# Optimization experiments

Hardware: AMD Instinct MI355X
Metric: run time of the kernel (lower is better)

## Reference

```python
import jax, jax.numpy as jnp
import numpy as np

N, T, D, C = 32, 512, 1024, 120
EPS = 1e-12
SCALE = 2.0 * (D ** 0.5)


def setup_inputs() -> dict:
    key = jax.random.key(0)
    ks = jax.random.split(key, 16)
    inp = {
        'anc_perm_input': jax.random.normal(ks[0], (N, T, D), dtype=jnp.float32),
        'pos_perm_input': jax.random.normal(ks[1], (N, T, D), dtype=jnp.float32),
        'neg_perm_input': jax.random.normal(ks[2], (N, T, D), dtype=jnp.float32),
        'anc_src_key_padding_mask': jax.random.randint(ks[3], (N, T), 0, 2) == 1,
        'pos_src_key_padding_mask': jax.random.randint(ks[4], (N, T), 0, 2) == 1,
        'neg_src_key_padding_mask': jax.random.randint(ks[5], (N, T), 0, 2) == 1,
        # learned parameters (stored as (in, out); math-equivalent to torch x @ W.T)
        'W_attn': jax.random.normal(ks[6], (D, D), dtype=jnp.float32) * 0.02,
        'b_attn': jnp.zeros((D,), dtype=jnp.float32),
        'W1': jax.random.normal(ks[7], (D, D), dtype=jnp.float32) * 0.02,
        'b1': jnp.zeros((D,), dtype=jnp.float32),
        'W2': jax.random.normal(ks[8], (D, D), dtype=jnp.float32) * 0.02,
        'b2': jnp.zeros((D,), dtype=jnp.float32),
        'ln_g': jnp.ones((D,), dtype=jnp.float32),
        'ln_b': jnp.zeros((D,), dtype=jnp.float32),
        'W_last': jax.random.normal(ks[9], (D, C), dtype=jnp.float32) * 0.02,
        'b_last': jnp.zeros((C,), dtype=jnp.float32),
    }
    return inp


def _ntd_nd(x, mask, W_attn, b_attn, W1, b1, W2, b2, ln_g, ln_b, W_last, b_last):
    # x: (N,T,D); mask: (N,T) bool, True = padding
    w = x @ W_attn + b_attn                                   # (N,T,D)
    valid = ~mask                                             # (N,T)
    scores = jnp.einsum('btd,bsd->bts', w, w)                 # (N,T,T)
    scores = jnp.where(valid[:, :, None] & valid[:, None, :], scores, 0.0)
    s = jnp.sum(scores, axis=1) / SCALE                       # (N,T)
    s = jnp.where(mask, -jnp.inf, s)
    attn = jax.nn.softmax(s, axis=1)                          # (N,T)
    # proj_head: duplicate OrderedDict key => linear1 -> relu -> linear2 (no final act)
    proj = jax.nn.relu(x @ W1 + b1) @ W2 + b2                 # (N,T,D)
    pooled = jnp.einsum('bt,btd->bd', attn, proj)             # (N,D)
    mu = jnp.mean(pooled, axis=-1, keepdims=True)
    var = jnp.var(pooled, axis=-1, keepdims=True)
    normed = (pooled - mu) / jnp.sqrt(var + EPS) * ln_g + ln_b
    return jax.nn.relu(normed) @ W_last + b_last              # (N,C)


def reference(anc_perm_input, pos_perm_input, neg_perm_input,
              anc_src_key_padding_mask, pos_src_key_padding_mask, neg_src_key_padding_mask,
              W_attn, b_attn, W1, b1, W2, b2, ln_g, ln_b, W_last, b_last):
    params = (W_attn, b_attn, W1, b1, W2, b2, ln_g, ln_b, W_last, b_last)
    anc = _ntd_nd(anc_perm_input, anc_src_key_padding_mask, *params)
    pos = _ntd_nd(pos_perm_input, pos_src_key_padding_mask, *params)
    neg = _ntd_nd(neg_perm_input, neg_src_key_padding_mask, *params)
    return (anc, pos, neg)
```

## Files before the change

kernel.cpp:

```cpp
#include <hip/hip_runtime.h>
#include <hip/hip_bf16.h>
#include <math.h>

#define N_B 32
#define T_S 512
#define D_D 1024
#define C_C 120
#define ZB 96
#define SCALE 64.0f

typedef unsigned short u16;
typedef __attribute__((ext_vector_type(8))) short short8;
typedef __attribute__((ext_vector_type(8))) unsigned short ushort8;
typedef __attribute__((ext_vector_type(4))) float floatx4;

__device__ inline u16 f2bf(float f) {
    union { __hip_bfloat16 h; u16 u; } c; c.h = __float2bfloat16(f); return c.u;
}
__device__ inline float bf2f(u16 u) {
    union { unsigned i; float f; } c; c.i = ((unsigned)u) << 16; return c.f;
}

__device__ inline void gll16(const void* g, void* l) {
    __builtin_amdgcn_global_load_lds((const __attribute__((address_space(1))) void*)g,
                                     (__attribute__((address_space(3))) void*)l,
                                     16, 0, 0);
}

__device__ inline bool mask_is_i8(const int* mk) {
    bool i8 = false;
#pragma unroll
    for (int i = 0; i < 16; i++) {
        unsigned v = ((const unsigned*)mk)[i];
        if (v > 1u) i8 = true;
    }
    return i8;
}
__device__ inline int mask_val(const int* mk, int idx, bool i8) {
    return i8 ? (int)((const signed char*)mk)[idx] : mk[idx];
}

__global__ void k_scan(const int* m0, const int* m1, const int* m2,
                       int* __restrict__ chunk_base, int* __restrict__ cnts,
                       u16* __restrict__ xp) {
    int zb = blockIdx.x;
    int z = zb >> 5, b = zb & 31;
    const int* mk = z == 0 ? m0 : (z == 1 ? m1 : m2);
    bool i8 = mask_is_i8(mk);
    int tid = threadIdx.x;
    __shared__ int wcnt[8];
    bool v0 = (mask_val(mk, b * T_S + tid, i8) == 0);
    bool v1 = (mask_val(mk, b * T_S + 256 + tid, i8) == 0);
    unsigned long long b0 = __ballot(v0);
    unsigned long long b1 = __ballot(v1);
    int wave = tid >> 6;
    if ((tid & 63) == 0) {
        wcnt[wave] = (int)__popcll(b0);
        wcnt[wave + 4] = (int)__popcll(b1);
    }
    __syncthreads();
    __shared__ int s_cnt;
    if (tid == 0) {
        int run = 0;
#pragma unroll
        for (int c = 0; c < 8; c++) {
            chunk_base[zb * 8 + c] = run;
            run += wcnt[c];
        }
        cnts[zb] = run;
        s_cnt = run;
    }
    __syncthreads();
    int cnt = s_cnt;
    int cend = (cnt + 127) & ~127;
    if (cend > T_S) cend = T_S;
    u16* base = xp + ((size_t)zb * T_S + cnt) * D_D;
    int n8 = (cend - cnt) * (D_D / 8);
    ushort8 zz = {0,0,0,0,0,0,0,0};
    for (int i = tid; i < n8; i += 256)
        *(ushort8*)(base + (size_t)i * 8) = zz;
}

__global__ void k_prep(const float* __restrict__ W_attn, const float* __restrict__ W1,
                       const float* x0, const float* x1, const float* x2,
                       const int* m0, const int* m1, const int* m2,
                       const int* __restrict__ chunk_base,
                       float* __restrict__ WT, u16* __restrict__ W1T,
                       float* __restrict__ xsum, u16* __restrict__ xp) {
    int bx = blockIdx.x;
    int tid = threadIdx.x;
    if (bx < 1024) {
        int tbx = bx & 31, tby = bx >> 5;
        __shared__ float tile[32][33];
        int tx = tid & 31, ty = tid >> 5;
#pragma unroll
        for (int j = 0; j < 32; j += 8)
            tile[ty + j][tx] = W_attn[(size_t)(tby*32 + ty + j)*D_D + tbx*32 + tx];
        __syncthreads();
#pragma unroll
        for (int j = 0; j < 32; j += 8)
            WT[(size_t)(tbx*32 + ty + j)*D_D + tby*32 + tx] = tile[tx][ty + j];
        __syncthreads();
#pragma unroll
        for (int j = 0; j < 32; j += 8)
            tile[ty + j][tx] = W1[(size_t)(tby*32 + ty + j)*D_D + tbx*32 + tx];
        __syncthreads();
#pragma unroll
        for (int j = 0; j < 32; j += 8)
            W1T[(size_t)(tbx*32 + ty + j)*D_D + tby*32 + tx] = f2bf(tile[tx][ty + j]);
        return;
    }
    int idx = bx - 1024;
    int chunk = idx & 7, zb = idx >> 3;
    int z = zb >> 5, b = zb & 31;
    const float* x = z == 0 ? x0 : (z == 1 ? x1 : x2);
    const int* mk = z == 0 ? m0 : (z == 1 ? m1 : m2);
    bool i8 = mask_is_i8(mk);
    int t0 = chunk * 64;
    int slot = chunk_base[zb * 8 + chunk];
    const float4* xr = (const float4*)(x + (size_t)(b * T_S) * D_D);
    u16* pack = xp + (size_t)zb * T_S * D_D;
    float4 acc = {0.f, 0.f, 0.f, 0.f};
    for (int i = 0; i < 64; i++) {
        int t = t0 + i;
        if (mask_val(mk, b * T_S + t, i8) == 0) {
            float4 v = xr[(size_t)t * 256 + tid];
            union { __hip_bfloat162 h; ushort2 u; } c0, c1;
            c0.h = __float22bfloat162_rn({v.x, v.y});
            c1.h = __float22bfloat162_rn({v.z, v.w});
            ushort4 uu = {c0.u.x, c0.u.y, c1.u.x, c1.u.y};
            *(ushort4*)(pack + (size_t)slot * D_D + tid * 4) = uu;
            slot++;
            acc.x += v.x; acc.y += v.y; acc.z += v.z; acc.w += v.w;
        }
    }
    float* xs = xsum + (size_t)zb * D_D + tid * 4;
    atomicAdd(xs + 0, acc.x); atomicAdd(xs + 1, acc.y);
    atomicAdd(xs + 2, acc.z); atomicAdd(xs + 3, acc.w);
}

__global__ void k_matvec(const float* __restrict__ W, const float* __restrict__ vin,
                         const float* __restrict__ bias, const int* __restrict__ bmul,
                         float scale, float* __restrict__ vout) {
    int z = blockIdx.z, bg = blockIdx.y;
    int och = blockIdx.x >> 3, kc = blockIdx.x & 7;
    int o = och * 256 + threadIdx.x;
    int brow = z * N_B + bg * 4;
    float acc[4] = {0.f, 0.f, 0.f, 0.f};
    if (kc == 0 && bias) {
        float bv = bias[o];
#pragma unroll
        for (int bb = 0; bb < 4; bb++)
            acc[bb] = bmul ? bv * (float)bmul[brow + bb] : bv;
    }
    const float* vi = vin + (size_t)brow * D_D + kc * 128;
    const float* Wp = W + (size_t)(kc * 128) * D_D + o;
#pragma unroll 4
    for (int i = 0; i < 128; i++) {
        float wv = Wp[(size_t)i * D_D];
#pragma unroll
        for (int bb = 0; bb < 4; bb++)
            acc[bb] += vi[(size_t)bb * D_D + i] * wv;
    }
#pragma unroll
    for (int bb = 0; bb < 4; bb++)
        atomicAdd(&vout[(size_t)(brow + bb) * D_D + o], acc[bb] * scale);
}

__global__ void k_dots(const u16* __restrict__ xp, const float* __restrict__ vs,
                       const int* __restrict__ cnts, float* __restrict__ sdot) {
    int zb = blockIdx.y;
    int t0 = blockIdx.x * 4;
    if (t0 >= cnts[zb]) return;
    int t = t0 + (threadIdx.x >> 6);
    int lane = threadIdx.x & 63;
    const u16* xr = xp + ((size_t)zb * T_S + t) * D_D;
    const float* vr = vs + (size_t)zb * D_D;
    float acc = 0.f;
#pragma unroll
    for (int i = 0; i < 2; i++) {
        short8 v = *(const short8*)(xr + i * 512 + lane * 8);
        const float* vp = vr + i * 512 + lane * 8;
        float4 a0 = *(const float4*)(vp);
        float4 a1 = *(const float4*)(vp + 4);
        acc += bf2f((u16)v[0]) * a0.x + bf2f((u16)v[1]) * a0.y
             + bf2f((u16)v[2]) * a0.z + bf2f((u16)v[3]) * a0.w
             + bf2f((u16)v[4]) * a1.x + bf2f((u16)v[5]) * a1.y
             + bf2f((u16)v[6]) * a1.z + bf2f((u16)v[7]) * a1.w;
    }
#pragma unroll
    for (int off = 32; off; off >>= 1) acc += __shfl_xor(acc, off, 64);
    if (lane == 0) sdot[(size_t)zb * T_S + t] = acc;
}

__global__ __launch_bounds__(256, 4)
void k_gemm_bf16(const u16* __restrict__ xp, const u16* __restrict__ W1T,
                 const float* __restrict__ b1, const float* __restrict__ sdot,
                 const int* __restrict__ cnts, float* __restrict__ r) {
    int flat = blockIdx.x;
    int low3 = flat & 7, xt = (flat >> 3) & 7;
    int g = ((flat >> 6) << 3) + low3;
    int tile = g & 3, zb = g >> 2;
    int row0 = tile * 128, N0 = xt * 128;
    int cnt = cnts[zb];
    if (row0 >= cnt) return;

    __shared__ __align__(16) u16 As[128 * 64];
    __shared__ __align__(16) u16 Bs[128 * 64];
    __shared__ float sAttn[128];
    __shared__ float redm[4], reds[4];
    int tid = threadIdx.x;
    int wave = tid >> 6, lane = tid & 63;

    {
        int base = zb * T_S;
        float v0 = (tid < cnt) ? sdot[base + tid] : -INFINITY;
        float v1 = (tid + 256 < cnt) ? sdot[base + 256 + tid] : -INFINITY;
        float mx = fmaxf(v0, v1);
#pragma unroll
        for (int off = 32; off; off >>= 1) mx = fmaxf(mx, __shfl_xor(mx, off, 64));
        if (lane == 0) redm[wave] = mx;
        __syncthreads();
        mx = fmaxf(fmaxf(redm[0], redm[1]), fmaxf(redm[2], redm[3]));
        float e = __expf(v0 - mx) + __expf(v1 - mx);
#pragma unroll
        for (int off = 32; off; off >>= 1) e += __shfl_xor(e, off, 64);
        if (lane == 0) reds[wave] = e;
        __syncthreads();
        float tot = reds[0] + reds[1] + reds[2] + reds[3];
        if (tid < 128) {
            int t = row0 + tid;
            float av = 0.f;
            if (t < cnt) av = __expf(sdot[base + t] - mx) / tot;
            sAttn[tid] = av;
        }
    }

    int wy = wave >> 1, wx = wave & 1;
    int q = lane >> 4, cidx = lane & 15;
    int srow = lane >> 3;
    int cp = lane & 7;

    floatx4 acc[4][4];
#pragma unroll
    for (int mi = 0; mi < 4; mi++)
#pragma unroll
        for (int ni = 0; ni < 4; ni++)
            acc[mi][ni] = (floatx4){0.f, 0.f, 0.f, 0.f};

    const u16* abase = xp + ((size_t)zb * T_S + row0) * D_D;
    const u16* bbase = W1T + (size_t)N0 * D_D;

    for (int k0 = 0; k0 < 1024; k0 += 64) {
        __syncthreads();
#pragma unroll
        for (int i = 0; i < 4; i++) {
            int r0 = wave * 32 + i * 8;
            int rr = r0 + srow;
            int gc = cp ^ (rr & 7);
            gll16(abase + (size_t)rr * D_D + k0 + gc * 8, &As[r0 * 64]);
        }
#pragma unroll
        for (int i = 0; i < 4; i++) {
            int r0 = wave * 32 + i * 8;
            int nn = r0 + srow;
            int gc = cp ^ (nn & 7);
            gll16(bbase + (size_t)nn * D_D + k0 + gc * 8, &Bs[r0 * 64]);
        }
        __syncthreads();
#pragma unroll
        for (int ks = 0; ks < 2; ks++) {
            short8 a[4], bfr[4];
#pragma unroll
            for (int mi = 0; mi < 4; mi++) {
                int m = wy * 64 + mi * 16 + cidx;
                a[mi] = *(const short8*)&As[m * 64 + (((ks << 2) | q) ^ (m & 7)) * 8];
            }
#pragma unroll
            for (int ni = 0; ni < 4; ni++) {
                int n = wx * 64 + ni * 16 + cidx;
                bfr[ni] = *(const short8*)&Bs[n * 64 + (((ks << 2) | q) ^ (n & 7)) * 8];
            }
#pragma unroll
            for (int mi = 0; mi < 4; mi++)
#pragma unroll
                for (int ni = 0; ni < 4; ni++)
                    acc[mi][ni] = __builtin_amdgcn_mfma_f32_16x16x32_bf16(
                        a[mi], bfr[ni], acc[mi][ni], 0, 0, 0);
        }
    }

    float* rrow = r + (size_t)zb * D_D;
#pragma unroll
    for (int ni = 0; ni < 4; ni++) {
        int ng = N0 + wx * 64 + ni * 16 + cidx;
        float b1v = b1[ng];
        float sum = 0.f;
#pragma unroll
        for (int mi = 0; mi < 4; mi++) {
#pragma unroll
            for (int rg = 0; rg < 4; rg++) {
                int ml = wy * 64 + mi * 16 + q * 4 + rg;
                float hv = acc[mi][ni][rg] + b1v;
                hv = fmaxf(hv, 0.f);
                sum += hv * sAttn[ml];
            }
        }
        sum += __shfl_xor(sum, 16, 64);
        sum += __shfl_xor(sum, 32, 64);
        if (lane < 16) atomicAdd(&rrow[ng], sum);
    }
}

__global__ void k_pool(const float* __restrict__ rbuf, const float* __restrict__ W2,
                       const float* __restrict__ b2, float* __restrict__ pooled) {
    int zb = blockIdx.y;
    int och = blockIdx.x >> 3, kc = blockIdx.x & 7;
    int o = och * 256 + threadIdx.x;
    float acc = (kc == 0) ? b2[o] : 0.f;
    const float* rp = rbuf + (size_t)zb * D_D + kc * 128;
    const float* Wp = W2 + (size_t)(kc * 128) * D_D + o;
#pragma unroll 4
    for (int i = 0; i < 128; i++)
        acc += rp[i] * Wp[(size_t)i * D_D];
    atomicAdd(&pooled[(size_t)zb * D_D + o], acc);
}

__global__ void k_fin(const float* __restrict__ pooled, const float* __restrict__ ln_g,
                      const float* __restrict__ ln_b, const float* __restrict__ Wl,
                      const float* __restrict__ bl, float* __restrict__ out) {
    int zb = blockIdx.x;
    int tid = threadIdx.x;
    __shared__ float nr[D_D];
    __shared__ float redA[8], redB[8];
    __shared__ float ps[4][C_C];
    const float* p = pooled + (size_t)zb * D_D;
    int o0 = tid, o1 = tid + 512;
    float a0 = p[o0], a1 = p[o1];
    float s1 = a0 + a1, s2 = a0 * a0 + a1 * a1;
#pragma unroll
    for (int off = 32; off; off >>= 1) {
        s1 += __shfl_xor(s1, off, 64);
        s2 += __shfl_xor(s2, off, 64);
    }
    int w = tid >> 6;
    if ((tid & 63) == 0) { redA[w] = s1; redB[w] = s2; }
    __syncthreads();
    float t1 = 0.f, t2 = 0.f;
#pragma unroll
    for (int k = 0; k < 8; k++) { t1 += redA[k]; t2 += redB[k]; }
    float mu = t1 * (1.0f / D_D);
    float var = t2 * (1.0f / D_D) - mu * mu;
    float rstd = 1.0f / sqrtf(var + 1e-12f);
    nr[o0] = fmaxf((a0 - mu) * rstd * ln_g[o0] + ln_b[o0], 0.f);
    nr[o1] = fmaxf((a1 - mu) * rstd * ln_g[o1] + ln_b[o1], 0.f);
    __syncthreads();
    if (tid < 4 * C_C) {
        int seg = tid / C_C, c = tid - seg * C_C;
        const float* wp = Wl + (size_t)(seg * 256) * C_C + c;
        const float* np = nr + seg * 256;
        float acc = 0.f;
#pragma unroll 8
        for (int d = 0; d < 256; d++)
            acc += np[d] * wp[(size_t)d * C_C];
        ps[seg][c] = acc;
    }
    __syncthreads();
    if (tid < C_C)
        out[(size_t)zb * C_C + tid] =
            bl[tid] + ps[0][tid] + ps[1][tid] + ps[2][tid] + ps[3][tid];
}

extern "C" void kernel_launch(void* const* d_in, const int* in_sizes, int n_in,
                              void* d_out, int out_size, void* d_ws, size_t ws_size,
                              hipStream_t stream) {
    const float* x0 = (const float*)d_in[0];
    const float* x1 = (const float*)d_in[1];
    const float* x2 = (const float*)d_in[2];
    const int* m0 = (const int*)d_in[3];
    const int* m1 = (const int*)d_in[4];
    const int* m2 = (const int*)d_in[5];
    const float* W_attn = (const float*)d_in[6];
    const float* b_attn = (const float*)d_in[7];
    const float* W1 = (const float*)d_in[8];
    const float* b1 = (const float*)d_in[9];
    const float* W2 = (const float*)d_in[10];
    const float* b2 = (const float*)d_in[11];
    const float* ln_g = (const float*)d_in[12];
    const float* ln_b = (const float*)d_in[13];
    const float* W_last = (const float*)d_in[14];
    const float* b_last = (const float*)d_in[15];
    float* out = (float*)d_out;

    char* wsb = (char*)d_ws;
    const size_t MB = 1 << 20;
    float* WT     = (float*)(wsb);
    u16*   W1T    = (u16*)  (wsb + 4 * MB);
    float* xsum   = (float*)(wsb + 6 * MB);
    float* rbuf   = (float*)(wsb + 6 * MB + 393216);
    float* wsum   = (float*)(wsb + 6 * MB + 786432);
    float* vs     = (float*)(wsb + 6 * MB + 1179648);
    float* pooled = (float*)(wsb + 6 * MB + 1572864);
    float* sdot   = (float*)(wsb + 8 * MB);
    int*   cbase  = (int*)  (wsb + 8 * MB + 196608);
    int*   cnts   = (int*)  (wsb + 8 * MB + 199680);
    u16*   xp     = (u16*)  (wsb + 9 * MB);

    hipMemsetAsync(wsb + 6 * MB, 0, 2 * MB, stream);

    k_scan  <<<ZB, 256, 0, stream>>>(m0, m1, m2, cbase, cnts, xp);
    k_prep  <<<1792, 256, 0, stream>>>(W_attn, W1, x0, x1, x2, m0, m1, m2,
                                       cbase, WT, W1T, xsum, xp);
    k_matvec<<<dim3(32, 8, 3), 256, 0, stream>>>(W_attn, xsum, b_attn, cnts, 1.0f, wsum);
    k_matvec<<<dim3(32, 8, 3), 256, 0, stream>>>(WT, wsum, nullptr, nullptr, 1.0f / SCALE, vs);
    k_dots  <<<dim3(128, ZB), 256, 0, stream>>>(xp, vs, cnts, sdot);
    k_gemm_bf16<<<3072, 256, 0, stream>>>(xp, W1T, b1, sdot, cnts, rbuf);
    k_pool  <<<dim3(32, ZB), 256, 0, stream>>>(rbuf, W2, b2, pooled);
    k_fin   <<<ZB, 512, 0, stream>>>(pooled, ln_g, ln_b, W_last, b_last, out);
}
```

Measured before the change: 404.9 us.

## Fuse W2 pooling projection into final layernorm kernel and relax GEMM launch bounds

Removes the separate split-K k_pool kernel with atomics and computes the W2 matvec inside the final per-batch kernel, staging the reduced row in shared memory. This drops one launch, the pooled buffer and atomic traffic. The fused kernel has only one block per batch row, and each thread runs a 1024-step loop over W2, so parallelism is much lower. The GEMM launch bound is also lowered to allow more registers per thread.

```diff
diff --git a/kernel.cpp b/kernel.cpp
--- a/kernel.cpp
+++ b/kernel.cpp
@@ -193,7 +193,7 @@
     if (lane == 0) sdot[(size_t)zb * T_S + t] = acc;
 }
 
-__global__ __launch_bounds__(256, 4)
+__global__ __launch_bounds__(256, 3)
 void k_gemm_bf16(const u16* __restrict__ xp, const u16* __restrict__ W1T,
                  const float* __restrict__ b1, const float* __restrict__ sdot,
                  const int* __restrict__ cnts, float* __restrict__ r) {
@@ -312,31 +312,28 @@
     }
 }
 
-__global__ void k_pool(const float* __restrict__ rbuf, const float* __restrict__ W2,
-                       const float* __restrict__ b2, float* __restrict__ pooled) {
-    int zb = blockIdx.y;
-    int och = blockIdx.x >> 3, kc = blockIdx.x & 7;
-    int o = och * 256 + threadIdx.x;
-    float acc = (kc == 0) ? b2[o] : 0.f;
-    const float* rp = rbuf + (size_t)zb * D_D + kc * 128;
-    const float* Wp = W2 + (size_t)(kc * 128) * D_D + o;
-#pragma unroll 4
-    for (int i = 0; i < 128; i++)
-        acc += rp[i] * Wp[(size_t)i * D_D];
-    atomicAdd(&pooled[(size_t)zb * D_D + o], acc);
-}
-
-__global__ void k_fin(const float* __restrict__ pooled, const float* __restrict__ ln_g,
-                      const float* __restrict__ ln_b, const float* __restrict__ Wl,
-                      const float* __restrict__ bl, float* __restrict__ out) {
+__global__ void k_tail(const float* __restrict__ rbuf, const float* __restrict__ W2,
+                       const float* __restrict__ b2, const float* __restrict__ ln_g,
+                       const float* __restrict__ ln_b, const float* __restrict__ Wl,
+                       const float* __restrict__ bl, float* __restrict__ out) {
     int zb = blockIdx.x;
     int tid = threadIdx.x;
+    __shared__ float rrow[D_D];
     __shared__ float nr[D_D];
     __shared__ float redA[8], redB[8];
     __shared__ float ps[4][C_C];
-    const float* p = pooled + (size_t)zb * D_D;
+    const float* rp = rbuf + (size_t)zb * D_D;
+    rrow[tid] = rp[tid];
+    rrow[tid + 512] = rp[tid + 512];
+    __syncthreads();
     int o0 = tid, o1 = tid + 512;
-    float a0 = p[o0], a1 = p[o1];
+    float a0 = b2[o0], a1 = b2[o1];
+#pragma unroll 8
+    for (int i = 0; i < D_D; i++) {
+        float rv = rrow[i];
+        a0 += rv * W2[(size_t)i * D_D + o0];
+        a1 += rv * W2[(size_t)i * D_D + o1];
+    }
     float s1 = a0 + a1, s2 = a0 * a0 + a1 * a1;
 #pragma unroll
     for (int off = 32; off; off >>= 1) {
@@ -400,7 +397,6 @@
     float* rbuf   = (float*)(wsb + 6 * MB + 393216);
     float* wsum   = (float*)(wsb + 6 * MB + 786432);
     float* vs     = (float*)(wsb + 6 * MB + 1179648);
-    float* pooled = (float*)(wsb + 6 * MB + 1572864);
     float* sdot   = (float*)(wsb + 8 * MB);
     int*   cbase  = (int*)  (wsb + 8 * MB + 196608);
     int*   cnts   = (int*)  (wsb + 8 * MB + 199680);
@@ -415,6 +411,5 @@
     k_matvec<<<dim3(32, 8, 3), 256, 0, stream>>>(WT, wsum, nullptr, nullptr, 1.0f / SCALE, vs);
     k_dots  <<<dim3(128, ZB), 256, 0, stream>>>(xp, vs, cnts, sdot);
     k_gemm_bf16<<<3072, 256, 0, stream>>>(xp, W1T, b1, sdot, cnts, rbuf);
-    k_pool  <<<dim3(32, ZB), 256, 0, stream>>>(rbuf, W2, b2, pooled);
-    k_fin   <<<ZB, 512, 0, stream>>>(pooled, ln_g, ln_b, W_last, b_last, out);
-}
+    k_tail  <<<ZB, 512, 0, stream>>>(rbuf, W2, b2, ln_g, ln_b, W_last, b_last, out);
+}
```

Result: slower. 438.7 us (+8.4%).

## Double-buffer bf16 GEMM LDS loads and pack valid rows via index list

Applied to the files above, without the earlier changes.

The bf16 GEMM now double-buffers its A/B LDS tiles, issuing the next k-slice's global-to-LDS loads before computing the current one with explicit vmcnt waits, and drops occupancy bounds to 2 waves per SIMD to fit the doubled shared memory. The mask scan now emits a compacted source-index list, so the packing kernel iterates only over valid rows instead of testing every timestep's mask. The weight transpose is split into its own kernel. This trades occupancy for load/compute overlap and adds a launch.

```diff
diff --git a/kernel.cpp b/kernel.cpp
--- a/kernel.cpp
+++ b/kernel.cpp
@@ -41,36 +41,36 @@
 }
 
 __global__ void k_scan(const int* m0, const int* m1, const int* m2,
-                       int* __restrict__ chunk_base, int* __restrict__ cnts,
+                       int* __restrict__ srcidx, int* __restrict__ cnts,
                        u16* __restrict__ xp) {
     int zb = blockIdx.x;
     int z = zb >> 5, b = zb & 31;
     const int* mk = z == 0 ? m0 : (z == 1 ? m1 : m2);
     bool i8 = mask_is_i8(mk);
     int tid = threadIdx.x;
-    __shared__ int wcnt[8];
+    __shared__ unsigned long long smask[8];
+    __shared__ int cbase[8];
+    __shared__ int s_cnt;
     bool v0 = (mask_val(mk, b * T_S + tid, i8) == 0);
     bool v1 = (mask_val(mk, b * T_S + 256 + tid, i8) == 0);
     unsigned long long b0 = __ballot(v0);
     unsigned long long b1 = __ballot(v1);
-    int wave = tid >> 6;
-    if ((tid & 63) == 0) {
-        wcnt[wave] = (int)__popcll(b0);
-        wcnt[wave + 4] = (int)__popcll(b1);
-    }
-    __syncthreads();
-    __shared__ int s_cnt;
+    int wave = tid >> 6, lane = tid & 63;
+    if (lane == 0) { smask[wave] = b0; smask[wave + 4] = b1; }
+    __syncthreads();
     if (tid == 0) {
         int run = 0;
 #pragma unroll
-        for (int c = 0; c < 8; c++) {
-            chunk_base[zb * 8 + c] = run;
-            run += wcnt[c];
-        }
+        for (int c = 0; c < 8; c++) { cbase[c] = run; run += (int)__popcll(smask[c]); }
         cnts[zb] = run;
         s_cnt = run;
     }
     __syncthreads();
+    unsigned long long lanemask = (lane == 63) ? ~0ull >> 1 : ((1ull << (lane + 1)) - 1) >> 1;
+    lanemask = (lane == 0) ? 0ull : ((1ull << lane) - 1);
+    int c0 = wave, c1 = wave + 4;
+    if (v0) srcidx[zb * T_S + cbase[c0] + (int)__popcll(smask[c0] & lanemask)] = tid;
+    if (v1) srcidx[zb * T_S + cbase[c1] + (int)__popcll(smask[c1] & lanemask)] = tid + 256;
     int cnt = s_cnt;
     int cend = (cnt + 127) & ~127;
     if (cend > T_S) cend = T_S;
@@ -81,58 +81,55 @@
         *(ushort8*)(base + (size_t)i * 8) = zz;
 }
 
-__global__ void k_prep(const float* __restrict__ W_attn, const float* __restrict__ W1,
-                       const float* x0, const float* x1, const float* x2,
-                       const int* m0, const int* m1, const int* m2,
-                       const int* __restrict__ chunk_base,
-                       float* __restrict__ WT, u16* __restrict__ W1T,
-                       float* __restrict__ xsum, u16* __restrict__ xp) {
+__global__ void k_trans(const float* __restrict__ W_attn, const float* __restrict__ W1,
+                        float* __restrict__ WT, u16* __restrict__ W1T) {
     int bx = blockIdx.x;
     int tid = threadIdx.x;
-    if (bx < 1024) {
-        int tbx = bx & 31, tby = bx >> 5;
-        __shared__ float tile[32][33];
-        int tx = tid & 31, ty = tid >> 5;
-#pragma unroll
-        for (int j = 0; j < 32; j += 8)
-            tile[ty + j][tx] = W_attn[(size_t)(tby*32 + ty + j)*D_D + tbx*32 + tx];
-        __syncthreads();
-#pragma unroll
-        for (int j = 0; j < 32; j += 8)
-            WT[(size_t)(tbx*32 + ty + j)*D_D + tby*32 + tx] = tile[tx][ty + j];
-        __syncthreads();
-#pragma unroll
-        for (int j = 0; j < 32; j += 8)
-            tile[ty + j][tx] = W1[(size_t)(tby*32 + ty + j)*D_D + tbx*32 + tx];
-        __syncthreads();
-#pragma unroll
-        for (int j = 0; j < 32; j += 8)
-            W1T[(size_t)(tbx*32 + ty + j)*D_D + tby*32 + tx] = f2bf(tile[tx][ty + j]);
-        return;
-    }
-    int idx = bx - 1024;
-    int chunk = idx & 7, zb = idx >> 3;
+    int tbx = bx & 31, tby = bx >> 5;
+    __shared__ float tile[32][33];
+    int tx = tid & 31, ty = tid >> 5;
+#pragma unroll
+    for (int j = 0; j < 32; j += 8)
+        tile[ty + j][tx] = W_attn[(size_t)(tby*32 + ty + j)*D_D + tbx*32 + tx];
+    __syncthreads();
+#pragma unroll
+    for (int j = 0; j < 32; j += 8)
+        WT[(size_t)(tbx*32 + ty + j)*D_D + tby*32 + tx] = tile[tx][ty + j];
+    __syncthreads();
+#pragma unroll
+    for (int j = 0; j < 32; j += 8)
+        tile[ty + j][tx] = W1[(size_t)(tby*32 + ty + j)*D_D + tbx*32 + tx];
+    __syncthreads();
+#pragma unroll
+    for (int j = 0; j < 32; j += 8)
+        W1T[(size_t)(tbx*32 + ty + j)*D_D + tby*32 + tx] = f2bf(tile[tx][ty + j]);
+}
+
+__global__ void k_pack(const float* x0, const float* x1, const float* x2,
+                       const int* __restrict__ srcidx, const int* __restrict__ cnts,
+                       float* __restrict__ xsum, u16* __restrict__ xp) {
+    int zb = blockIdx.y;
+    int s0 = blockIdx.x * 64;
+    int cnt = cnts[zb];
+    if (s0 >= cnt) return;
+    int m = cnt - s0; if (m > 64) m = 64;
     int z = zb >> 5, b = zb & 31;
     const float* x = z == 0 ? x0 : (z == 1 ? x1 : x2);
-    const int* mk = z == 0 ? m0 : (z == 1 ? m1 : m2);
-    bool i8 = mask_is_i8(mk);
-    int t0 = chunk * 64;
-    int slot = chunk_base[zb * 8 + chunk];
-    const float4* xr = (const float4*)(x + (size_t)(b * T_S) * D_D);
-    u16* pack = xp + (size_t)zb * T_S * D_D;
+    int tid = threadIdx.x;
+    const float* xrow = x + (size_t)(b * T_S) * D_D;
+    u16* pack = xp + ((size_t)zb * T_S + s0) * D_D;
+    const int* si = srcidx + zb * T_S + s0;
     float4 acc = {0.f, 0.f, 0.f, 0.f};
-    for (int i = 0; i < 64; i++) {
-        int t = t0 + i;
-        if (mask_val(mk, b * T_S + t, i8) == 0) {
-            float4 v = xr[(size_t)t * 256 + tid];
-            union { __hip_bfloat162 h; ushort2 u; } c0, c1;
-            c0.h = __float22bfloat162_rn({v.x, v.y});
-            c1.h = __float22bfloat162_rn({v.z, v.w});
-            ushort4 uu = {c0.u.x, c0.u.y, c1.u.x, c1.u.y};
-            *(ushort4*)(pack + (size_t)slot * D_D + tid * 4) = uu;
-            slot++;
-            acc.x += v.x; acc.y += v.y; acc.z += v.z; acc.w += v.w;
-        }
+#pragma unroll 4
+    for (int i = 0; i < m; i++) {
+        int t = si[i];
+        float4 v = *(const float4*)(xrow + (size_t)t * D_D + tid * 4);
+        union { __hip_bfloat162 h; ushort2 u; } c0, c1;
+        c0.h = __float22bfloat162_rn({v.x, v.y});
+        c1.h = __float22bfloat162_rn({v.z, v.w});
+        ushort4 uu = {c0.u.x, c0.u.y, c1.u.x, c1.u.y};
+        *(ushort4*)(pack + (size_t)i * D_D + tid * 4) = uu;
+        acc.x += v.x; acc.y += v.y; acc.z += v.z; acc.w += v.w;
     }
     float* xs = xsum + (size_t)zb * D_D + tid * 4;
     atomicAdd(xs + 0, acc.x); atomicAdd(xs + 1, acc.y);
@@ -193,7 +190,7 @@
     if (lane == 0) sdot[(size_t)zb * T_S + t] = acc;
 }
 
-__global__ __launch_bounds__(256, 4)
+__global__ __launch_bounds__(256, 2)
 void k_gemm_bf16(const u16* __restrict__ xp, const u16* __restrict__ W1T,
                  const float* __restrict__ b1, const float* __restrict__ sdot,
                  const int* __restrict__ cnts, float* __restrict__ r) {
@@ -205,8 +202,8 @@
     int cnt = cnts[zb];
     if (row0 >= cnt) return;
 
-    __shared__ __align__(16) u16 As[128 * 64];
-    __shared__ __align__(16) u16 Bs[128 * 64];
+    __shared__ __align__(16) u16 As[2][128 * 64];
+    __shared__ __align__(16) u16 Bs[2][128 * 64];
     __shared__ float sAttn[128];
     __shared__ float redm[4], reds[4];
     int tid = threadIdx.x;
@@ -234,6 +231,7 @@
             if (t < cnt) av = __expf(sdot[base + t] - mx) / tot;
             sAttn[tid] = av;
         }
+        __syncthreads();
     }
 
     int wy = wave >> 1, wx = wave & 1;
@@ -251,35 +249,44 @@
     const u16* abase = xp + ((size_t)zb * T_S + row0) * D_D;
     const u16* bbase = W1T + (size_t)N0 * D_D;
 
-    for (int k0 = 0; k0 < 1024; k0 += 64) {
-        __syncthreads();
+    auto stage = [&](int k0, int buf) {
 #pragma unroll
         for (int i = 0; i < 4; i++) {
             int r0 = wave * 32 + i * 8;
             int rr = r0 + srow;
             int gc = cp ^ (rr & 7);
-            gll16(abase + (size_t)rr * D_D + k0 + gc * 8, &As[r0 * 64]);
+            gll16(abase + (size_t)rr * D_D + k0 + gc * 8, &As[buf][r0 * 64]);
         }
 #pragma unroll
         for (int i = 0; i < 4; i++) {
             int r0 = wave * 32 + i * 8;
             int nn = r0 + srow;
             int gc = cp ^ (nn & 7);
-            gll16(bbase + (size_t)nn * D_D + k0 + gc * 8, &Bs[r0 * 64]);
-        }
-        __syncthreads();
+            gll16(bbase + (size_t)nn * D_D + k0 + gc * 8, &Bs[buf][r0 * 64]);
+        }
+    };
+
+    stage(0, 0);
+    for (int k = 0; k < 16; k++) {
+        int buf = k & 1;
+        if (k < 15) {
+            stage((k + 1) * 64, buf ^ 1);
+            asm volatile("s_waitcnt vmcnt(8)\n\ts_barrier" ::: "memory");
+        } else {
+            asm volatile("s_waitcnt vmcnt(0)\n\ts_barrier" ::: "memory");
+        }
 #pragma unroll
         for (int ks = 0; ks < 2; ks++) {
             short8 a[4], bfr[4];
 #pragma unroll
             for (int mi = 0; mi < 4; mi++) {
-                int m = wy * 64 + mi * 16 + cidx;
-                a[mi] = *(const short8*)&As[m * 64 + (((ks << 2) | q) ^ (m & 7)) * 8];
+                int mr = wy * 64 + mi * 16 + cidx;
+                a[mi] = *(const short8*)&As[buf][mr * 64 + (((ks << 2) | q) ^ (mr & 7)) * 8];
             }
 #pragma unroll
             for (int ni = 0; ni < 4; ni++) {
                 int n = wx * 64 + ni * 16 + cidx;
-                bfr[ni] = *(const short8*)&Bs[n * 64 + (((ks << 2) | q) ^ (n & 7)) * 8];
+                bfr[ni] = *(const short8*)&Bs[buf][n * 64 + (((ks << 2) | q) ^ (n & 7)) * 8];
             }
 #pragma unroll
             for (int mi = 0; mi < 4; mi++)
@@ -288,6 +295,7 @@
                     acc[mi][ni] = __builtin_amdgcn_mfma_f32_16x16x32_bf16(
                         a[mi], bfr[ni], acc[mi][ni], 0, 0, 0);
         }
+        asm volatile("s_waitcnt lgkmcnt(0)\n\ts_barrier" ::: "memory");
     }
 
     float* rrow = r + (size_t)zb * D_D;
@@ -402,15 +410,15 @@
     float* vs     = (float*)(wsb + 6 * MB + 1179648);
     float* pooled = (float*)(wsb + 6 * MB + 1572864);
     float* sdot   = (float*)(wsb + 8 * MB);
-    int*   cbase  = (int*)  (wsb + 8 * MB + 196608);
-    int*   cnts   = (int*)  (wsb + 8 * MB + 199680);
+    int*   cnts   = (int*)  (wsb + 8 * MB + 196608);
+    int*   srcidx = (int*)  (wsb + 8 * MB + 200704);
     u16*   xp     = (u16*)  (wsb + 9 * MB);
 
     hipMemsetAsync(wsb + 6 * MB, 0, 2 * MB, stream);
 
-    k_scan  <<<ZB, 256, 0, stream>>>(m0, m1, m2, cbase, cnts, xp);
-    k_prep  <<<1792, 256, 0, stream>>>(W_attn, W1, x0, x1, x2, m0, m1, m2,
-                                       cbase, WT, W1T, xsum, xp);
+    k_scan  <<<ZB, 256, 0, stream>>>(m0, m1, m2, srcidx, cnts, xp);
+    k_trans <<<1024, 256, 0, stream>>>(W_attn, W1, WT, W1T);
+    k_pack  <<<dim3(8, ZB), 256, 0, stream>>>(x0, x1, x2, srcidx, cnts, xsum, xp);
     k_matvec<<<dim3(32, 8, 3), 256, 0, stream>>>(W_attn, xsum, b_attn, cnts, 1.0f, wsum);
     k_matvec<<<dim3(32, 8, 3), 256, 0, stream>>>(WT, wsum, nullptr, nullptr, 1.0f / SCALE, vs);
     k_dots  <<<dim3(128, ZB), 256, 0, stream>>>(xp, vs, cnts, sdot);
```

Result: slower. 423.5 us (+4.6%).
